# Optimization experiments

Hardware: AMD Instinct MI355X
Metric: run time of the kernel (lower is better)

## Reference

```python
import jax, jax.numpy as jnp
import numpy as np
from jax import lax

C, K, EMB = 10, 32, 32
B, H, W = 32, 128, 128
DIRS = ((-1, 0), (1, 0), (0, -1), (0, 1))  # up, down, left, right


def _shift(x, dh, dw):
    # shift (B,H,W,...) by (dh,dw) with zero fill; x[b,h,w] <- x[b,h+dh,w+dw]
    pad = [(0, 0), (max(dh, 0), max(-dh, 0)), (max(dw, 0), max(-dw, 0))] + [(0, 0)] * (x.ndim - 3)
    xp = jnp.pad(x, pad)
    h0, w0 = max(-dh, 0), max(-dw, 0)
    return lax.dynamic_slice_in_dim(lax.dynamic_slice_in_dim(xp, h0, x.shape[1], 1), w0, x.shape[2], 2)


def conv(x, w, b):
    y = lax.conv_general_dilated(x, w, (1, 1), 'SAME',
                                 dimension_numbers=('NHWC', 'HWIO', 'NHWC'))
    return y + b


def small_cnn(x, w1, b1, w2, b2, w3, b3):
    x = jax.nn.relu(conv(x, w1, b1))
    x = jax.nn.relu(conv(x, w2, b2))
    return conv(x, w3, b3)


def neighbor_affinity(phi, tau=0.5):
    # phi: (B,H,W,D) -> w: (B,H,W,4) Gaussian feature affinity to 4 neighbors
    ones = jnp.ones(phi.shape[:3] + (1,), phi.dtype)
    ws = []
    for dh, dw in DIRS:
        nb = _shift(phi, dh, dw)
        valid = _shift(ones, dh, dw)[..., 0]
        d2 = jnp.sum((phi - nb) ** 2, axis=-1)
        ws.append(jnp.exp(-d2 / tau) * valid)
    return jnp.stack(ws, axis=-1)


def init_seeds_soft(Bv, Hv, Wv, Kv, dtype=jnp.float32):
    # K seeds on a gh x gw grid; soft assignment by squared distance
    gh = 4
    gw = Kv // gh
    sh = (jnp.arange(gh, dtype=dtype) + 0.5) * (Hv / gh)
    sw = (jnp.arange(gw, dtype=dtype) + 0.5) * (Wv / gw)
    seed_h = jnp.repeat(sh, gw)  # (K,)
    seed_w = jnp.tile(sw, gh)    # (K,)
    hh = jnp.arange(Hv, dtype=dtype)[:, None, None]
    ww = jnp.arange(Wv, dtype=dtype)[None, :, None]
    d2 = (hh - seed_h) ** 2 + (ww - seed_w) ** 2  # (H,W,K)
    sigma2 = (Hv / gh) * (Wv / gw)
    A = jax.nn.softmax(-d2 / sigma2, axis=-1)
    return jnp.broadcast_to(A[None], (Bv, Hv, Wv, Kv))


def soft_message_pass(A, w, beta=2.0):
    # aggregate neighbor assignments weighted by affinity, renormalize over K
    agg = jnp.zeros_like(A)
    for d, (dh, dw) in enumerate(DIRS):
        agg = agg + w[..., d:d + 1] * _shift(A, dh, dw)
    return jax.nn.softmax(beta * agg, axis=-1)


def soft_pool_features(G, A):
    # G:(B,H,W,C), A:(B,H,W,K) -> T:(B,K,1+2+C+4)
    Bv, Hv, Wv, Cv = G.shape
    eps = 1e-6
    mass = jnp.sum(A, axis=(1, 2)) + eps                      # (B,K)
    hh = (jnp.arange(Hv, dtype=G.dtype) + 0.5) / Hv
    ww = (jnp.arange(Wv, dtype=G.dtype) + 0.5) / Wv
    h_c = jnp.einsum('bhwk,h->bk', A, hh) / mass
    w_c = jnp.einsum('bhwk,w->bk', A, ww) / mass
    col = jnp.einsum('bhwk,bhwc->bkc', A, G) / mass[..., None]
    h2 = jnp.einsum('bhwk,h->bk', A, hh ** 2) / mass
    w2 = jnp.einsum('bhwk,w->bk', A, ww ** 2) / mass
    h_sd = jnp.sqrt(jax.nn.relu(h2 - h_c ** 2) + eps)
    w_sd = jnp.sqrt(jax.nn.relu(w2 - w_c ** 2) + eps)
    size = (mass / (Hv * Wv))[..., None]                      # (B,K,1)
    cen = jnp.stack([h_c, w_c], axis=-1)                      # (B,K,2)
    bbox = jnp.stack([h_c - h_sd, h_c + h_sd, w_c - w_sd, w_c + w_sd], axis=-1)
    return jnp.concatenate([size, cen, col, bbox], axis=-1)


def setup_inputs() -> dict:
    key = jax.random.key(0)
    ks = jax.random.split(key, 4)
    X = jax.random.randint(ks[0], (B, H, W), 0, C)
    w1 = jax.random.normal(ks[1], (3, 3, C, 32), jnp.float32) * (1.0 / np.sqrt(9 * C))
    w2 = jax.random.normal(ks[2], (3, 3, 32, 32), jnp.float32) * (1.0 / np.sqrt(9 * 32))
    w3 = jax.random.normal(ks[3], (1, 1, 32, EMB), jnp.float32) * (1.0 / np.sqrt(32))
    return {'X': X, 'w1': w1, 'b1': jnp.zeros((32,), jnp.float32),
            'w2': w2, 'b2': jnp.zeros((32,), jnp.float32),
            'w3': w3, 'b3': jnp.zeros((EMB,), jnp.float32)}


def reference(X, w1, b1, w2, b2, w3, b3):
    G = jax.nn.one_hot(X, C, dtype=jnp.float32)              # (B,H,W,C)
    phi = small_cnn(G, w1, b1, w2, b2, w3, b3)               # (B,H,W,EMB)
    w = neighbor_affinity(phi)                               # (B,H,W,4)
    A = init_seeds_soft(G.shape[0], G.shape[1], G.shape[2], K, G.dtype)
    for _ in range(8):
        A = soft_message_pass(A, w, beta=2.0)
    T = soft_pool_features(G, A)
    return A, T
```

## Files before the change

kernel.cpp:

```cpp
#include <hip/hip_runtime.h>
#include <math.h>

#define HD 128
#define WD 128
#define BB 32
#define KK 32
#define NPIX (BB*HD*WD)
#define PLANE ((size_t)NPIX*8)

typedef _Float16 f16;
typedef __attribute__((ext_vector_type(8))) _Float16 f16x8;
typedef __attribute__((ext_vector_type(4))) float f32x4;

__device__ __forceinline__ int swz(int row, int g){
  return row*64 + (((g + (row >> 1)) & 3) << 4);
}

__device__ __forceinline__ float xexp2(float x){
#if __has_builtin(__builtin_amdgcn_exp2f)
  return __builtin_amdgcn_exp2f(x);
#else
  return exp2f(x);
#endif
}
__device__ __forceinline__ float xrcp(float x){
#if __has_builtin(__builtin_amdgcn_rcpf)
  return __builtin_amdgcn_rcpf(x);
#else
  return 1.f/x;
#endif
}
__device__ __forceinline__ f16x8 bc8(f16 x){
  f16x8 v;
  #pragma unroll
  for (int j = 0; j < 8; j++) v[j] = x;
  return v;
}

__global__ __launch_bounds__(512, 2) void cnn_kernel(
    const int* __restrict__ X,
    const float* __restrict__ w1, const float* __restrict__ b1,
    const float* __restrict__ w2, const float* __restrict__ b2,
    const float* __restrict__ w3, const float* __restrict__ b3,
    f16* __restrict__ phi)
{
  __shared__ f16 sW1f[9*11*40];
  __shared__ int   sX[20*36];
  __shared__ float sB2[32], sB3[32];
  __shared__ f16 x1[612*32];
  __shared__ f16 w2t[9*32*32];
  __shared__ f16 w3t[32*32];

  const int tid = threadIdx.x;
  const int img = blockIdx.z;
  const int bh0 = blockIdx.y * 16;
  const int bw0 = blockIdx.x * 32;

  for (int i = tid; i < 9*11*32; i += 512) {
    int tap = i / 352, c = (i % 352) >> 5, oc = i & 31;
    float v = (c < 10) ? w1[tap*320 + c*32 + oc] : 0.f;
    if (tap == 4 && c < 10) v += b1[oc];
    sW1f[(tap*11 + c)*40 + oc] = (f16)v;
  }
  for (int i = tid; i < 9*32*32; i += 512) {
    int tap = i >> 10, ic = (i >> 5) & 31, oc = i & 31;
    int off = swz(tap*32 + oc, ic >> 3) + (ic & 7)*2;
    *(f16*)((char*)w2t + off) = (f16)w2[i];
  }
  for (int i = tid; i < 32*32; i += 512) {
    int ic = i >> 5, oe = i & 31;
    int off = swz(oe, ic >> 3) + (ic & 7)*2;
    *(f16*)((char*)w3t + off) = (f16)w3[i];
  }
  if (tid < 32) { sB2[tid] = b2[tid]; sB3[tid] = b3[tid]; }
  for (int i = tid; i < 20*36; i += 512) {
    int ti = i / 36, tj = i % 36;
    int gh = bh0 - 2 + ti, gw = bw0 - 2 + tj;
    sX[i] = (gh >= 0 && gh < HD && gw >= 0 && gw < WD) ? X[(img*HD + gh)*WD + gw] : 10;
  }
  __syncthreads();

  for (int p = tid; p < 612; p += 512) {
    int hr = p / 34, hc = p - hr*34;
    int gh = bh0 + hr - 1, gw = bw0 + hc - 1;
    if (gh >= 0 && gh < HD && gw >= 0 && gw < WD) {
      f16x8 acc[4];
      {
        int c = sX[hr*36 + hc];
        const f16* wr = &sW1f[c*40];
        #pragma unroll
        for (int g = 0; g < 4; g++) acc[g] = *(const f16x8*)(wr + g*8);
      }
      #pragma unroll
      for (int tap = 1; tap < 9; tap++) {
        const int ti = tap/3, tj = tap%3;
        int c = sX[(hr+ti)*36 + hc + tj];
        const f16* wr = &sW1f[(tap*11 + c)*40];
        #pragma unroll
        for (int g = 0; g < 4; g++) acc[g] += *(const f16x8*)(wr + g*8);
      }
      #pragma unroll
      for (int g = 0; g < 4; g++) {
        f16x8 r = acc[g];
        #pragma unroll
        for (int j = 0; j < 8; j++) r[j] = (r[j] > (f16)0.f) ? r[j] : (f16)0.f;
        *(f16x8*)((char*)x1 + swz(p, g)) = r;
      }
    } else {
      f16x8 z;
      #pragma unroll
      for (int j = 0; j < 8; j++) z[j] = (f16)0.f;
      #pragma unroll
      for (int g = 0; g < 4; g++) *(f16x8*)((char*)x1 + swz(p, g)) = z;
    }
  }
  __syncthreads();

  const int lane = tid & 63;
  const int wv   = tid >> 6;
  const int lr   = lane & 15;
  const int kg   = lane >> 4;
  const int mts  = wv * 4;

  int arow0[4];
  #pragma unroll
  for (int q = 0; q < 4; q++) {
    int px = (mts + q)*16 + lr;
    arow0[q] = (px >> 5)*34 + (px & 31);
  }
  float b2v0 = sB2[lr], b2v1 = sB2[lr + 16];
  f32x4 acc[4][2];
  #pragma unroll
  for (int q = 0; q < 4; q++) {
    acc[q][0] = (f32x4){b2v0, b2v0, b2v0, b2v0};
    acc[q][1] = (f32x4){b2v1, b2v1, b2v1, b2v1};
  }
  #pragma unroll
  for (int tap = 0; tap < 9; tap++) {
    const int ti = tap/3, tj = tap%3;
    f16x8 bf0 = *(const f16x8*)((const char*)w2t + swz(tap*32 + lr,      kg));
    f16x8 bf1 = *(const f16x8*)((const char*)w2t + swz(tap*32 + lr + 16, kg));
    #pragma unroll
    for (int q = 0; q < 4; q++) {
      int row = arow0[q] + ti*34 + tj;
      f16x8 af = *(const f16x8*)((const char*)x1 + swz(row, kg));
      acc[q][0] = __builtin_amdgcn_mfma_f32_16x16x32_f16(af, bf0, acc[q][0], 0, 0, 0);
      acc[q][1] = __builtin_amdgcn_mfma_f32_16x16x32_f16(af, bf1, acc[q][1], 0, 0, 0);
    }
  }
  __syncthreads();

  #pragma unroll
  for (int q = 0; q < 4; q++)
    #pragma unroll
    for (int nt = 0; nt < 2; nt++) {
      int oc = nt*16 + lr;
      #pragma unroll
      for (int rg = 0; rg < 4; rg++) {
        int px = (mts + q)*16 + kg*4 + rg;
        int off = swz(px, oc >> 3) + (oc & 7)*2;
        *(f16*)((char*)x1 + off) = (f16)fmaxf(acc[q][nt][rg], 0.f);
      }
    }
  __syncthreads();

  {
    f16x8 cf0 = *(const f16x8*)((const char*)w3t + swz(lr,      kg));
    f16x8 cf1 = *(const f16x8*)((const char*)w3t + swz(lr + 16, kg));
    float b3v0 = sB3[lr], b3v1 = sB3[lr + 16];
    #pragma unroll
    for (int q = 0; q < 4; q++) {
      f16x8 af = *(const f16x8*)((const char*)x1 + swz((mts + q)*16 + lr, kg));
      f32x4 o0 = (f32x4){b3v0, b3v0, b3v0, b3v0};
      f32x4 o1 = (f32x4){b3v1, b3v1, b3v1, b3v1};
      o0 = __builtin_amdgcn_mfma_f32_16x16x32_f16(af, cf0, o0, 0, 0, 0);
      o1 = __builtin_amdgcn_mfma_f32_16x16x32_f16(af, cf1, o1, 0, 0, 0);
      #pragma unroll
      for (int rg = 0; rg < 4; rg++) {
        int px = (mts + q)*16 + kg*4 + rg;
        int gh = bh0 + (px >> 5), gw = bw0 + (px & 31);
        f16* dst = phi + ((size_t)((img*HD + gh)*WD + gw))*32;
        dst[lr]      = (f16)o0[rg];
        dst[lr + 16] = (f16)o1[rg];
      }
    }
  }
}

#define WSCALE 2.8853900817779268f

__device__ __forceinline__ float aff_lds(const f16* __restrict__ sphi, int slot,
                                         f16x8 c0, f16x8 c1, f16x8 c2, f16x8 c3,
                                         bool valid) {
  f16x8 n0 = *(const f16x8*)((const char*)sphi + swz(slot, 0));
  f16x8 n1 = *(const f16x8*)((const char*)sphi + swz(slot, 1));
  f16x8 n2 = *(const f16x8*)((const char*)sphi + swz(slot, 2));
  f16x8 n3 = *(const f16x8*)((const char*)sphi + swz(slot, 3));
  f16x8 d0 = c0 - n0; f16x8 s = d0*d0;
  f16x8 d1 = c1 - n1; s += d1*d1;
  f16x8 d2 = c2 - n2; s += d2*d2;
  f16x8 d3 = c3 - n3; s += d3*d3;
  float d2f = 0.f;
  #pragma unroll
  for (int j = 0; j < 8; j++) d2f += (float)s[j];
  return valid ? WSCALE * xexp2(-WSCALE * d2f) : 0.f;
}

__global__ __launch_bounds__(256, 4) void aff_kernel(const f16* __restrict__ phi, float* __restrict__ wb) {
  __shared__ f16 sphi[612*32];

  const int blk  = blockIdx.x;
  const int tile = blk & 31;
  const int img  = blk >> 5;
  const int th0  = (tile >> 2) * 16;
  const int tw0  = (tile & 3) * 32;
  const size_t ibase = (size_t)img * HD * WD;

  for (int task = threadIdx.x; task < 2448; task += 256) {
    int p = task >> 2, g = task & 3;
    int r = p / 34, c = p - r*34;
    int gh = min(max(th0 - 1 + r, 0), HD-1);
    int gw = min(max(tw0 - 1 + c, 0), WD-1);
    f16x8 v = *(const f16x8*)(phi + (ibase + gh*WD + gw)*32 + g*8);
    *(f16x8*)((char*)sphi + swz(p, g)) = v;
  }
  __syncthreads();

  for (int p2 = threadIdx.x; p2 < 512; p2 += 256) {
    int r2 = p2 >> 5, c2 = p2 & 31;
    int gh = th0 + r2, gw = tw0 + c2;
    int qc = (r2+1)*34 + (c2+1);
    f16x8 c0 = *(const f16x8*)((const char*)sphi + swz(qc, 0));
    f16x8 c1 = *(const f16x8*)((const char*)sphi + swz(qc, 1));
    f16x8 c2v = *(const f16x8*)((const char*)sphi + swz(qc, 2));
    f16x8 c3 = *(const f16x8*)((const char*)sphi + swz(qc, 3));
    float4 out;
    out.x = aff_lds(sphi, qc + 34, c0,c1,c2v,c3, gh < HD-1);
    out.y = aff_lds(sphi, qc - 34, c0,c1,c2v,c3, gh > 0);
    out.z = aff_lds(sphi, qc + 1,  c0,c1,c2v,c3, gw < WD-1);
    out.w = aff_lds(sphi, qc - 1,  c0,c1,c2v,c3, gw > 0);
    ((float4*)wb)[ibase + gh*WD + gw] = out;
  }
}

__device__ __forceinline__ void a0_accum2(float* a, int hh, int ww, float wt) {
  const float C = 0.0028177637517362567f;
  float eh[4], ew[8];
  float sh = 0.f, sw = 0.f;
  const float fh = (float)hh, fw = (float)ww;
  #pragma unroll
  for (int kh = 0; kh < 4; kh++) { float d = fh - (float)(kh*32+16); eh[kh] = xexp2(-d*d*C); sh += eh[kh]; }
  #pragma unroll
  for (int kw = 0; kw < 8; kw++) { float d = fw - (float)(kw*16+8); ew[kw] = xexp2(-d*d*C); sw += ew[kw]; }
  float sc = wt * xrcp(sh * sw);
  #pragma unroll
  for (int kh = 0; kh < 4; kh++) {
    float ehs = eh[kh] * sc;
    #pragma unroll
    for (int kw = 0; kw < 8; kw++) a[kh*8+kw] = fmaf(ehs, ew[kw], a[kh*8+kw]);
  }
}

template<int FIRST>
__global__ __launch_bounds__(256, 6) void mp2_kernel(const f16* __restrict__ Ain,
                                                     const float* __restrict__ wb,
                                                     f16* __restrict__ Aout) {
  __shared__ f16 amid[340*32];

  const int blk  = blockIdx.x;
  const int xcd  = blk & 7;
  const int q    = blk >> 3;
  const int img  = xcd + ((q >> 6) << 3);
  const int tile = q & 63;
  const int th0  = (tile >> 2) * 8;
  const int tw0  = (tile & 3) * 32;
  const size_t ibase = (size_t)img * HD * WD;

  for (int p = threadIdx.x; p < 340; p += 256) {
    int r = p / 34, cc = p - r*34;
    int gh = th0 - 1 + r, gw = tw0 - 1 + cc;
    bool inimg = ((unsigned)gh < (unsigned)HD) && ((unsigned)gw < (unsigned)WD);
    int ghc = min(max(gh, 0), HD-1), gwc = min(max(gw, 0), WD-1);
    float4 wd = inimg ? ((const float4*)wb)[ibase + gh*WD + gw] : make_float4(0.f,0.f,0.f,0.f);
    int hu = ghc + ((ghc < HD-1) ? 1 : 0);
    int hd = ghc - ((ghc > 0)    ? 1 : 0);
    int wl = gwc + ((gwc < WD-1) ? 1 : 0);
    int wr = gwc - ((gwc > 0)    ? 1 : 0);

    float s = 0.f;
    f16x8 pe[4];
    if (FIRST) {
      float a[32];
      #pragma unroll
      for (int k = 0; k < 32; k++) a[k] = 0.f;
      a0_accum2(a, hu, gwc, wd.x);
      a0_accum2(a, hd, gwc, wd.y);
      a0_accum2(a, ghc, wl, wd.z);
      a0_accum2(a, ghc, wr, wd.w);
      #pragma unroll
      for (int g = 0; g < 4; g++)
        #pragma unroll
        for (int j = 0; j < 8; j++) { float e = xexp2(a[g*8+j]); s += e; pe[g][j] = (f16)e; }
    } else {
      const size_t iu_ = ibase + (size_t)hu*WD + gwc;
      const size_t id_ = ibase + (size_t)hd*WD + gwc;
      const size_t il_ = ibase + (size_t)ghc*WD + wl;
      const size_t ir_ = ibase + (size_t)ghc*WD + wr;
      f16x8 w0 = bc8((f16)wd.x), w1 = bc8((f16)wd.y), w2 = bc8((f16)wd.z), w3 = bc8((f16)wd.w);
      #pragma unroll
      for (int g = 0; g < 4; g++) {
        const f16* pg = Ain + (size_t)g*PLANE;
        f16x8 v0 = *(const f16x8*)(pg + iu_*8);
        f16x8 v1 = *(const f16x8*)(pg + id_*8);
        f16x8 v2 = *(const f16x8*)(pg + il_*8);
        f16x8 v3 = *(const f16x8*)(pg + ir_*8);
        f16x8 agg = v0*w0 + v1*w1 + v2*w2 + v3*w3;
        #pragma unroll
        for (int j = 0; j < 8; j++) { float e = xexp2((float)agg[j]); s += e; pe[g][j] = (f16)e; }
      }
    }
    f16x8 iv = bc8((f16)xrcp(s));
    #pragma unroll
    for (int g = 0; g < 4; g++)
      *(f16x8*)((char*)amid + swz(p, g)) = pe[g]*iv;
  }
  __syncthreads();

  {
    int r2 = threadIdx.x >> 5, c2 = threadIdx.x & 31;
    int gh = th0 + r2, gw = tw0 + c2;
    int rm = r2 + 1, cm = c2 + 1;
    float4 wd = ((const float4*)wb)[ibase + gh*WD + gw];
    int q0 = (rm + ((gh < HD-1) ? 1 : 0))*34 + cm;
    int q1 = (rm - ((gh > 0)    ? 1 : 0))*34 + cm;
    int q2 = rm*34 + cm + ((gw < WD-1) ? 1 : 0);
    int q3 = rm*34 + cm - ((gw > 0)    ? 1 : 0);
    f16x8 w0 = bc8((f16)wd.x), w1 = bc8((f16)wd.y), w2 = bc8((f16)wd.z), w3 = bc8((f16)wd.w);
    float s = 0.f;
    f16x8 pe[4];
    #pragma unroll
    for (int g = 0; g < 4; g++) {
      f16x8 v0 = *(const f16x8*)((const char*)amid + swz(q0, g));
      f16x8 v1 = *(const f16x8*)((const char*)amid + swz(q1, g));
      f16x8 v2 = *(const f16x8*)((const char*)amid + swz(q2, g));
      f16x8 v3 = *(const f16x8*)((const char*)amid + swz(q3, g));
      f16x8 agg = v0*w0 + v1*w1 + v2*w2 + v3*w3;
      #pragma unroll
      for (int j = 0; j < 8; j++) { float e = xexp2((float)agg[j]); s += e; pe[g][j] = (f16)e; }
    }
    f16x8 iv = bc8((f16)xrcp(s));
    size_t opix = ibase + (size_t)gh*WD + gw;
    #pragma unroll
    for (int g = 0; g < 4; g++)
      *(f16x8*)(Aout + (size_t)g*PLANE + opix*8) = pe[g]*iv;
  }
}

__global__ __launch_bounds__(256) void conv_kernel(const f16* __restrict__ Ap,
                                                   float* __restrict__ Aout) {
  const int t = blockIdx.x * 256 + threadIdx.x;
  const int px = t >> 2, g = t & 3;
  f16x8 v = *(const f16x8*)(Ap + (size_t)g*PLANE + (size_t)px*8);
  float4 o0, o1;
  o0.x = (float)v[0]; o0.y = (float)v[1]; o0.z = (float)v[2]; o0.w = (float)v[3];
  o1.x = (float)v[4]; o1.y = (float)v[5]; o1.z = (float)v[6]; o1.w = (float)v[7];
  float4* dst = (float4*)(Aout + (size_t)px*32 + g*8);
  dst[0] = o0; dst[1] = o1;
}

__global__ __launch_bounds__(256) void pool1_kernel(const f16* __restrict__ Ap,
                                                    const int* __restrict__ X,
                                                    float* __restrict__ part) {
  const int b = blockIdx.x, cy = blockIdx.y;
  const int k = threadIdx.x & 31, sub = threadIdx.x >> 5;
  const int h = cy*4 + (sub >> 1);
  const int w0 = (sub & 1) * 64;
  const float hh = ((float)h + 0.5f) * (1.f/128.f);
  float s0 = 0.f, sw = 0.f, sw2 = 0.f;
  float col[10];
  #pragma unroll
  for (int c = 0; c < 10; c++) col[c] = 0.f;
  const f16* pl = Ap + (size_t)(k >> 3)*PLANE + ((size_t)((b*HD + h)*WD + w0))*8 + (k & 7);
  const int* Xrow = X + (b*HD + h)*WD + w0;
  for (int w = 0; w < 64; w++) {
    float a  = (float)pl[w*8];
    float ww = ((float)(w + w0) + 0.5f) * (1.f/128.f);
    s0 += a; sw = fmaf(ww, a, sw); sw2 = fmaf(ww*ww, a, sw2);
    int x = Xrow[w];
    #pragma unroll
    for (int c = 0; c < 10; c++) col[c] += (x == c) ? a : 0.f;
  }
  __shared__ float red[8][32][15];
  float vals[15];
  vals[0] = s0; vals[1] = hh*s0; vals[2] = sw; vals[3] = hh*hh*s0; vals[4] = sw2;
  #pragma unroll
  for (int c = 0; c < 10; c++) vals[5+c] = col[c];
  #pragma unroll
  for (int q = 0; q < 15; q++) red[sub][k][q] = vals[q];
  __syncthreads();
  if (sub == 0) {
    #pragma unroll
    for (int q = 0; q < 15; q++) {
      float v = 0.f;
      #pragma unroll
      for (int s2 = 0; s2 < 8; s2++) v += red[s2][k][q];
      part[(((size_t)b*32 + cy)*32 + k)*15 + q] = v;
    }
  }
}

__global__ __launch_bounds__(256) void pool2_kernel(const float* __restrict__ part,
                                                    float* __restrict__ T) {
  const int t = blockIdx.x * 256 + threadIdx.x;
  if (t >= BB*KK) return;
  const int b = t >> 5, k = t & 31;
  float s[15];
  #pragma unroll
  for (int q = 0; q < 15; q++) s[q] = 0.f;
  for (int cy = 0; cy < 32; cy++) {
    const float* p = part + (((size_t)b*32 + cy)*32 + k)*15;
    #pragma unroll
    for (int q = 0; q < 15; q++) s[q] += p[q];
  }
  float mass = s[0] + 1e-6f;
  float inv  = 1.f / mass;
  float h_c = s[1]*inv, w_c = s[2]*inv, h2 = s[3]*inv, w2 = s[4]*inv;
  float h_sd = sqrtf(fmaxf(h2 - h_c*h_c, 0.f) + 1e-6f);
  float w_sd = sqrtf(fmaxf(w2 - w_c*w_c, 0.f) + 1e-6f);
  float* o = T + (size_t)t*17;
  o[0] = mass * (1.f/16384.f);
  o[1] = h_c; o[2] = w_c;
  #pragma unroll
  for (int c = 0; c < 10; c++) o[3+c] = s[5+c]*inv;
  o[13] = h_c - h_sd; o[14] = h_c + h_sd; o[15] = w_c - w_sd; o[16] = w_c + w_sd;
}

extern "C" void kernel_launch(void* const* d_in, const int* in_sizes, int n_in,
                              void* d_out, int out_size, void* d_ws, size_t ws_size,
                              hipStream_t stream) {
  const int*   X  = (const int*)d_in[0];
  const float* w1 = (const float*)d_in[1];
  const float* b1 = (const float*)d_in[2];
  const float* w2 = (const float*)d_in[3];
  const float* b2 = (const float*)d_in[4];
  const float* w3 = (const float*)d_in[5];
  const float* b3 = (const float*)d_in[6];

  float* out   = (float*)d_out;
  float* A_out = out;
  float* T_out = out + (size_t)NPIX * KK;

  char*  ws   = (char*)d_ws;
  f16*   bufA = (f16*)ws;
  f16*   bufB = (f16*)(ws + (size_t)32*1024*1024);
  float* wb   = (float*)(ws + (size_t)64*1024*1024);
  float* part = (float*)ws;

  f16* phi = bufB;
  cnn_kernel<<<dim3(WD/32, HD/16, BB), 512, 0, stream>>>(X, w1, b1, w2, b2, w3, b3, phi);
  aff_kernel<<<1024, 256, 0, stream>>>(phi, wb);

  mp2_kernel<1><<<2048, 256, 0, stream>>>(nullptr, wb, bufA);
  mp2_kernel<0><<<2048, 256, 0, stream>>>(bufA, wb, bufB);
  mp2_kernel<0><<<2048, 256, 0, stream>>>(bufB, wb, bufA);
  mp2_kernel<0><<<2048, 256, 0, stream>>>(bufA, wb, bufB);

  conv_kernel<<<NPIX*4/256, 256, 0, stream>>>(bufB, A_out);
  pool1_kernel<<<dim3(BB, 32), 256, 0, stream>>>(bufB, X, part);
  pool2_kernel<<<(BB*KK + 255)/256, 256, 0, stream>>>(part, T_out);
}
```

Before: 269.8 us.

## Fuse CNN with affinity, fuse fp32 output conversion into last message pass

```diff
diff --git a/kernel.cpp b/kernel.cpp
--- a/kernel.cpp
+++ b/kernel.cpp
@@ -10,6 +10,7 @@
 
 typedef _Float16 f16;
 typedef __attribute__((ext_vector_type(8))) _Float16 f16x8;
+typedef __attribute__((ext_vector_type(4))) _Float16 f16x4;
 typedef __attribute__((ext_vector_type(4))) float f32x4;
 
 __device__ __forceinline__ int swz(int row, int g){
@@ -37,17 +38,19 @@
   return v;
 }
 
-__global__ __launch_bounds__(512, 2) void cnn_kernel(
+#define WSCALE 2.8853900817779268f
+
+__global__ __launch_bounds__(512, 4) void cnnaff_kernel(
     const int* __restrict__ X,
     const float* __restrict__ w1, const float* __restrict__ b1,
     const float* __restrict__ w2, const float* __restrict__ b2,
     const float* __restrict__ w3, const float* __restrict__ b3,
-    f16* __restrict__ phi)
+    float* __restrict__ wb)
 {
   __shared__ f16 sW1f[9*11*40];
-  __shared__ int   sX[20*36];
+  __shared__ int   sX[22*38];
   __shared__ float sB2[32], sB3[32];
-  __shared__ f16 x1[612*32];
+  __shared__ f16 x1[720*32];
   __shared__ f16 w2t[9*32*32];
   __shared__ f16 w3t[32*32];
 
@@ -73,38 +76,38 @@
     *(f16*)((char*)w3t + off) = (f16)w3[i];
   }
   if (tid < 32) { sB2[tid] = b2[tid]; sB3[tid] = b3[tid]; }
-  for (int i = tid; i < 20*36; i += 512) {
-    int ti = i / 36, tj = i % 36;
-    int gh = bh0 - 2 + ti, gw = bw0 - 2 + tj;
+  for (int i = tid; i < 22*38; i += 512) {
+    int ti = i / 38, tj = i % 38;
+    int gh = bh0 - 3 + ti, gw = bw0 - 3 + tj;
     sX[i] = (gh >= 0 && gh < HD && gw >= 0 && gw < WD) ? X[(img*HD + gh)*WD + gw] : 10;
   }
   __syncthreads();
 
-  for (int p = tid; p < 612; p += 512) {
-    int hr = p / 34, hc = p - hr*34;
-    int gh = bh0 + hr - 1, gw = bw0 + hc - 1;
+  for (int p = tid; p < 720; p += 512) {
+    int r = p / 36, c = p - r*36;
+    int gh = bh0 - 2 + r, gw = bw0 - 2 + c;
     if (gh >= 0 && gh < HD && gw >= 0 && gw < WD) {
       f16x8 acc[4];
       {
-        int c = sX[hr*36 + hc];
-        const f16* wr = &sW1f[c*40];
+        int cc = sX[r*38 + c];
+        const f16* wr = &sW1f[cc*40];
         #pragma unroll
         for (int g = 0; g < 4; g++) acc[g] = *(const f16x8*)(wr + g*8);
       }
       #pragma unroll
       for (int tap = 1; tap < 9; tap++) {
         const int ti = tap/3, tj = tap%3;
-        int c = sX[(hr+ti)*36 + hc + tj];
-        const f16* wr = &sW1f[(tap*11 + c)*40];
+        int cc = sX[(r+ti)*38 + c + tj];
+        const f16* wr = &sW1f[(tap*11 + cc)*40];
         #pragma unroll
         for (int g = 0; g < 4; g++) acc[g] += *(const f16x8*)(wr + g*8);
       }
       #pragma unroll
       for (int g = 0; g < 4; g++) {
-        f16x8 r = acc[g];
+        f16x8 rr = acc[g];
         #pragma unroll
-        for (int j = 0; j < 8; j++) r[j] = (r[j] > (f16)0.f) ? r[j] : (f16)0.f;
-        *(f16x8*)((char*)x1 + swz(p, g)) = r;
+        for (int j = 0; j < 8; j++) rr[j] = (rr[j] > (f16)0.f) ? rr[j] : (f16)0.f;
+        *(f16x8*)((char*)x1 + swz(p, g)) = rr;
       }
     } else {
       f16x8 z;
@@ -120,18 +123,19 @@
   const int wv   = tid >> 6;
   const int lr   = lane & 15;
   const int kg   = lane >> 4;
-  const int mts  = wv * 4;
-
-  int arow0[4];
-  #pragma unroll
-  for (int q = 0; q < 4; q++) {
+  const int mts  = wv * 5;
+
+  int arow0[5];
+  #pragma unroll
+  for (int q = 0; q < 5; q++) {
     int px = (mts + q)*16 + lr;
-    arow0[q] = (px >> 5)*34 + (px & 31);
+    int pr = px / 34, pc = px - pr*34;
+    arow0[q] = pr*36 + pc;
   }
   float b2v0 = sB2[lr], b2v1 = sB2[lr + 16];
-  f32x4 acc[4][2];
-  #pragma unroll
-  for (int q = 0; q < 4; q++) {
+  f32x4 acc[5][2];
+  #pragma unroll
+  for (int q = 0; q < 5; q++) {
     acc[q][0] = (f32x4){b2v0, b2v0, b2v0, b2v0};
     acc[q][1] = (f32x4){b2v1, b2v1, b2v1, b2v1};
   }
@@ -141,8 +145,8 @@
     f16x8 bf0 = *(const f16x8*)((const char*)w2t + swz(tap*32 + lr,      kg));
     f16x8 bf1 = *(const f16x8*)((const char*)w2t + swz(tap*32 + lr + 16, kg));
     #pragma unroll
-    for (int q = 0; q < 4; q++) {
-      int row = arow0[q] + ti*34 + tj;
+    for (int q = 0; q < 5; q++) {
+      int row = arow0[q] + ti*36 + tj;
       f16x8 af = *(const f16x8*)((const char*)x1 + swz(row, kg));
       acc[q][0] = __builtin_amdgcn_mfma_f32_16x16x32_f16(af, bf0, acc[q][0], 0, 0, 0);
       acc[q][1] = __builtin_amdgcn_mfma_f32_16x16x32_f16(af, bf1, acc[q][1], 0, 0, 0);
@@ -151,7 +155,7 @@
   __syncthreads();
 
   #pragma unroll
-  for (int q = 0; q < 4; q++)
+  for (int q = 0; q < 5; q++)
     #pragma unroll
     for (int nt = 0; nt < 2; nt++) {
       int oc = nt*16 + lr;
@@ -169,7 +173,7 @@
     f16x8 cf1 = *(const f16x8*)((const char*)w3t + swz(lr + 16, kg));
     float b3v0 = sB3[lr], b3v1 = sB3[lr + 16];
     #pragma unroll
-    for (int q = 0; q < 4; q++) {
+    for (int q = 0; q < 5; q++) {
       f16x8 af = *(const f16x8*)((const char*)x1 + swz((mts + q)*16 + lr, kg));
       f32x4 o0 = (f32x4){b3v0, b3v0, b3v0, b3v0};
       f32x4 o1 = (f32x4){b3v1, b3v1, b3v1, b3v1};
@@ -178,68 +182,43 @@
       #pragma unroll
       for (int rg = 0; rg < 4; rg++) {
         int px = (mts + q)*16 + kg*4 + rg;
-        int gh = bh0 + (px >> 5), gw = bw0 + (px & 31);
-        f16* dst = phi + ((size_t)((img*HD + gh)*WD + gw))*32;
-        dst[lr]      = (f16)o0[rg];
-        dst[lr + 16] = (f16)o1[rg];
-      }
-    }
-  }
-}
-
-#define WSCALE 2.8853900817779268f
-
-__device__ __forceinline__ float aff_lds(const f16* __restrict__ sphi, int slot,
-                                         f16x8 c0, f16x8 c1, f16x8 c2, f16x8 c3,
-                                         bool valid) {
-  f16x8 n0 = *(const f16x8*)((const char*)sphi + swz(slot, 0));
-  f16x8 n1 = *(const f16x8*)((const char*)sphi + swz(slot, 1));
-  f16x8 n2 = *(const f16x8*)((const char*)sphi + swz(slot, 2));
-  f16x8 n3 = *(const f16x8*)((const char*)sphi + swz(slot, 3));
-  f16x8 d0 = c0 - n0; f16x8 s = d0*d0;
-  f16x8 d1 = c1 - n1; s += d1*d1;
-  f16x8 d2 = c2 - n2; s += d2*d2;
-  f16x8 d3 = c3 - n3; s += d3*d3;
-  float d2f = 0.f;
-  #pragma unroll
-  for (int j = 0; j < 8; j++) d2f += (float)s[j];
-  return valid ? WSCALE * xexp2(-WSCALE * d2f) : 0.f;
-}
-
-__global__ __launch_bounds__(256, 4) void aff_kernel(const f16* __restrict__ phi, float* __restrict__ wb) {
-  __shared__ f16 sphi[612*32];
-
-  const int blk  = blockIdx.x;
-  const int tile = blk & 31;
-  const int img  = blk >> 5;
-  const int th0  = (tile >> 2) * 16;
-  const int tw0  = (tile & 3) * 32;
-  const size_t ibase = (size_t)img * HD * WD;
-
-  for (int task = threadIdx.x; task < 2448; task += 256) {
-    int p = task >> 2, g = task & 3;
-    int r = p / 34, c = p - r*34;
-    int gh = min(max(th0 - 1 + r, 0), HD-1);
-    int gw = min(max(tw0 - 1 + c, 0), WD-1);
-    f16x8 v = *(const f16x8*)(phi + (ibase + gh*WD + gw)*32 + g*8);
-    *(f16x8*)((char*)sphi + swz(p, g)) = v;
-  }
-  __syncthreads();
-
-  for (int p2 = threadIdx.x; p2 < 512; p2 += 256) {
-    int r2 = p2 >> 5, c2 = p2 & 31;
-    int gh = th0 + r2, gw = tw0 + c2;
+        int offA = swz(px, lr >> 3) + (lr & 7)*2;
+        int offB = swz(px, (lr+16) >> 3) + (lr & 7)*2;
+        *(f16*)((char*)x1 + offA) = (f16)o0[rg];
+        *(f16*)((char*)x1 + offB) = (f16)o1[rg];
+      }
+    }
+  }
+  __syncthreads();
+
+  {
+    int r2 = tid >> 5, c2 = tid & 31;
+    int gh = bh0 + r2, gw = bw0 + c2;
     int qc = (r2+1)*34 + (c2+1);
-    f16x8 c0 = *(const f16x8*)((const char*)sphi + swz(qc, 0));
-    f16x8 c1 = *(const f16x8*)((const char*)sphi + swz(qc, 1));
-    f16x8 c2v = *(const f16x8*)((const char*)sphi + swz(qc, 2));
-    f16x8 c3 = *(const f16x8*)((const char*)sphi + swz(qc, 3));
+    f16x8 c0 = *(const f16x8*)((const char*)x1 + swz(qc, 0));
+    f16x8 c1 = *(const f16x8*)((const char*)x1 + swz(qc, 1));
+    f16x8 c2v = *(const f16x8*)((const char*)x1 + swz(qc, 2));
+    f16x8 c3 = *(const f16x8*)((const char*)x1 + swz(qc, 3));
     float4 out;
-    out.x = aff_lds(sphi, qc + 34, c0,c1,c2v,c3, gh < HD-1);
-    out.y = aff_lds(sphi, qc - 34, c0,c1,c2v,c3, gh > 0);
-    out.z = aff_lds(sphi, qc + 1,  c0,c1,c2v,c3, gw < WD-1);
-    out.w = aff_lds(sphi, qc - 1,  c0,c1,c2v,c3, gw > 0);
-    ((float4*)wb)[ibase + gh*WD + gw] = out;
+    #pragma unroll
+    for (int d = 0; d < 4; d++) {
+      int slot = (d == 0) ? qc + 34 : (d == 1) ? qc - 34 : (d == 2) ? qc + 1 : qc - 1;
+      bool valid = (d == 0) ? (gh < HD-1) : (d == 1) ? (gh > 0) : (d == 2) ? (gw < WD-1) : (gw > 0);
+      f16x8 n0 = *(const f16x8*)((const char*)x1 + swz(slot, 0));
+      f16x8 n1 = *(const f16x8*)((const char*)x1 + swz(slot, 1));
+      f16x8 n2 = *(const f16x8*)((const char*)x1 + swz(slot, 2));
+      f16x8 n3 = *(const f16x8*)((const char*)x1 + swz(slot, 3));
+      f16x8 d0 = c0 - n0; f16x8 s = d0*d0;
+      f16x8 d1 = c1 - n1; s += d1*d1;
+      f16x8 d2 = c2v - n2; s += d2*d2;
+      f16x8 d3 = c3 - n3; s += d3*d3;
+      float d2f = 0.f;
+      #pragma unroll
+      for (int j = 0; j < 8; j++) d2f += (float)s[j];
+      float v = valid ? WSCALE * xexp2(-WSCALE * d2f) : 0.f;
+      if (d == 0) out.x = v; else if (d == 1) out.y = v; else if (d == 2) out.z = v; else out.w = v;
+    }
+    ((float4*)wb)[(size_t)img*HD*WD + gh*WD + gw] = out;
   }
 }
 
@@ -261,22 +240,23 @@
   }
 }
 
-template<int FIRST>
-__global__ __launch_bounds__(256, 6) void mp2_kernel(const f16* __restrict__ Ain,
+template<int FIRST, int LAST>
+__global__ __launch_bounds__(512, 6) void mp2_kernel(const f16* __restrict__ Ain,
                                                      const float* __restrict__ wb,
-                                                     f16* __restrict__ Aout) {
-  __shared__ f16 amid[340*32];
+                                                     f16* __restrict__ Aout,
+                                                     float* __restrict__ AoutF) {
+  __shared__ f16 amid[612*32];
 
   const int blk  = blockIdx.x;
   const int xcd  = blk & 7;
   const int q    = blk >> 3;
-  const int img  = xcd + ((q >> 6) << 3);
-  const int tile = q & 63;
-  const int th0  = (tile >> 2) * 8;
+  const int img  = xcd + ((q >> 5) << 3);
+  const int tile = q & 31;
+  const int th0  = (tile >> 2) * 16;
   const int tw0  = (tile & 3) * 32;
   const size_t ibase = (size_t)img * HD * WD;
 
-  for (int p = threadIdx.x; p < 340; p += 256) {
+  for (int p = threadIdx.x; p < 612; p += 512) {
     int r = p / 34, cc = p - r*34;
     int gh = th0 - 1 + r, gw = tw0 - 1 + cc;
     bool inimg = ((unsigned)gh < (unsigned)HD) && ((unsigned)gw < (unsigned)WD);
@@ -349,26 +329,41 @@
       for (int j = 0; j < 8; j++) { float e = xexp2((float)agg[j]); s += e; pe[g][j] = (f16)e; }
     }
     f16x8 iv = bc8((f16)xrcp(s));
-    size_t opix = ibase + (size_t)gh*WD + gw;
-    #pragma unroll
-    for (int g = 0; g < 4; g++)
-      *(f16x8*)(Aout + (size_t)g*PLANE + opix*8) = pe[g]*iv;
-  }
-}
-
-__global__ __launch_bounds__(256) void conv_kernel(const f16* __restrict__ Ap,
-                                                   float* __restrict__ Aout) {
-  const int t = blockIdx.x * 256 + threadIdx.x;
-  const int px = t >> 2, g = t & 3;
-  f16x8 v = *(const f16x8*)(Ap + (size_t)g*PLANE + (size_t)px*8);
-  float4 o0, o1;
-  o0.x = (float)v[0]; o0.y = (float)v[1]; o0.z = (float)v[2]; o0.w = (float)v[3];
-  o1.x = (float)v[4]; o1.y = (float)v[5]; o1.z = (float)v[6]; o1.w = (float)v[7];
-  float4* dst = (float4*)(Aout + (size_t)px*32 + g*8);
-  dst[0] = o0; dst[1] = o1;
-}
-
-__global__ __launch_bounds__(256) void pool1_kernel(const f16* __restrict__ Ap,
+    #pragma unroll
+    for (int g = 0; g < 4; g++) pe[g] = pe[g]*iv;
+
+    if (!LAST) {
+      size_t opix = ibase + (size_t)gh*WD + gw;
+      #pragma unroll
+      for (int g = 0; g < 4; g++)
+        *(f16x8*)(Aout + (size_t)g*PLANE + opix*8) = pe[g];
+    } else {
+      __syncthreads();
+      f16* planes = amid;
+      #pragma unroll
+      for (int g = 0; g < 4; g++)
+        *(f16x8*)((char*)planes + (g*513 + threadIdx.x)*16) = pe[g];
+      __syncthreads();
+      float* obase = AoutF + ((size_t)(img*HD + th0)*WD + tw0)*32;
+      #pragma unroll
+      for (int rep = 0; rep < 8; rep++) {
+        int flat = rep*512 + threadIdx.x;
+        int row = flat >> 8;
+        int within = flat & 255;
+        int pxr = within >> 3;
+        int kq = within & 7;
+        int g = kq >> 1, half = kq & 1;
+        int pxl = row*32 + pxr;
+        f16x4 v = *(const f16x4*)((const char*)planes + (g*513 + pxl)*16 + half*8);
+        float4 o;
+        o.x = (float)v[0]; o.y = (float)v[1]; o.z = (float)v[2]; o.w = (float)v[3];
+        *(float4*)(obase + (size_t)row*WD*32 + pxr*32 + kq*4) = o;
+      }
+    }
+  }
+}
+
+__global__ __launch_bounds__(256) void pool1_kernel(const float* __restrict__ A,
                                                     const int* __restrict__ X,
                                                     float* __restrict__ part) {
   const int b = blockIdx.x, cy = blockIdx.y;
@@ -380,10 +375,10 @@
   float col[10];
   #pragma unroll
   for (int c = 0; c < 10; c++) col[c] = 0.f;
-  const f16* pl = Ap + (size_t)(k >> 3)*PLANE + ((size_t)((b*HD + h)*WD + w0))*8 + (k & 7);
-  const int* Xrow = X + (b*HD + h)*WD + w0;
+  const float* Arow = A + ((size_t)((b*HD + h)*WD + w0))*32 + k;
+  const int*   Xrow = X + (b*HD + h)*WD + w0;
   for (int w = 0; w < 64; w++) {
-    float a  = (float)pl[w*8];
+    float a  = Arow[(size_t)w*32];
     float ww = ((float)(w + w0) + 0.5f) * (1.f/128.f);
     s0 += a; sw = fmaf(ww, a, sw); sw2 = fmaf(ww*ww, a, sw2);
     int x = Xrow[w];
@@ -456,16 +451,13 @@
   float* wb   = (float*)(ws + (size_t)64*1024*1024);
   float* part = (float*)ws;
 
-  f16* phi = bufB;
-  cnn_kernel<<<dim3(WD/32, HD/16, BB), 512, 0, stream>>>(X, w1, b1, w2, b2, w3, b3, phi);
-  aff_kernel<<<1024, 256, 0, stream>>>(phi, wb);
-
-  mp2_kernel<1><<<2048, 256, 0, stream>>>(nullptr, wb, bufA);
-  mp2_kernel<0><<<2048, 256, 0, stream>>>(bufA, wb, bufB);
-  mp2_kernel<0><<<2048, 256, 0, stream>>>(bufB, wb, bufA);
-  mp2_kernel<0><<<2048, 256, 0, stream>>>(bufA, wb, bufB);
-
-  conv_kernel<<<NPIX*4/256, 256, 0, stream>>>(bufB, A_out);
-  pool1_kernel<<<dim3(BB, 32), 256, 0, stream>>>(bufB, X, part);
+  cnnaff_kernel<<<dim3(WD/32, HD/16, BB), 512, 0, stream>>>(X, w1, b1, w2, b2, w3, b3, wb);
+
+  mp2_kernel<1,0><<<1024, 512, 0, stream>>>(nullptr, wb, bufA, nullptr);
+  mp2_kernel<0,0><<<1024, 512, 0, stream>>>(bufA, wb, bufB, nullptr);
+  mp2_kernel<0,0><<<1024, 512, 0, stream>>>(bufB, wb, bufA, nullptr);
+  mp2_kernel<0,1><<<1024, 512, 0, stream>>>(bufA, wb, nullptr, A_out);
+
+  pool1_kernel<<<dim3(BB, 32), 256, 0, stream>>>(A_out, X, part);
   pool2_kernel<<<(BB*KK + 255)/256, 256, 0, stream>>>(part, T_out);
 }
```

Result: faster. 236.2 us (-12.5%).

## Fuse final message pass with fp32 output conversion and pooling partials

Applied to the files above, without the earlier changes.

```diff
diff --git a/kernel.cpp b/kernel.cpp
--- a/kernel.cpp
+++ b/kernel.cpp
@@ -10,6 +10,7 @@
 
 typedef _Float16 f16;
 typedef __attribute__((ext_vector_type(8))) _Float16 f16x8;
+typedef __attribute__((ext_vector_type(4))) _Float16 f16x4;
 typedef __attribute__((ext_vector_type(4))) float f32x4;
 
 __device__ __forceinline__ int swz(int row, int g){
@@ -36,6 +37,8 @@
   for (int j = 0; j < 8; j++) v[j] = x;
   return v;
 }
+
+#define WSCALE 2.8853900817779268f
 
 __global__ __launch_bounds__(512, 2) void cnn_kernel(
     const int* __restrict__ X,
@@ -186,8 +189,6 @@
     }
   }
 }
-
-#define WSCALE 2.8853900817779268f
 
 __device__ __forceinline__ float aff_lds(const f16* __restrict__ sphi, int slot,
                                          f16x8 c0, f16x8 c1, f16x8 c2, f16x8 c3,
@@ -262,21 +263,21 @@
 }
 
 template<int FIRST>
-__global__ __launch_bounds__(256, 6) void mp2_kernel(const f16* __restrict__ Ain,
+__global__ __launch_bounds__(512, 6) void mp2_kernel(const f16* __restrict__ Ain,
                                                      const float* __restrict__ wb,
                                                      f16* __restrict__ Aout) {
-  __shared__ f16 amid[340*32];
+  __shared__ f16 amid[612*32];
 
   const int blk  = blockIdx.x;
   const int xcd  = blk & 7;
   const int q    = blk >> 3;
-  const int img  = xcd + ((q >> 6) << 3);
-  const int tile = q & 63;
-  const int th0  = (tile >> 2) * 8;
+  const int img  = xcd + ((q >> 5) << 3);
+  const int tile = q & 31;
+  const int th0  = (tile >> 2) * 16;
   const int tw0  = (tile & 3) * 32;
   const size_t ibase = (size_t)img * HD * WD;
 
-  for (int p = threadIdx.x; p < 340; p += 256) {
+  for (int p = threadIdx.x; p < 612; p += 512) {
     int r = p / 34, cc = p - r*34;
     int gh = th0 - 1 + r, gw = tw0 - 1 + cc;
     bool inimg = ((unsigned)gh < (unsigned)HD) && ((unsigned)gw < (unsigned)WD);
@@ -356,56 +357,147 @@
   }
 }
 
-__global__ __launch_bounds__(256) void conv_kernel(const f16* __restrict__ Ap,
-                                                   float* __restrict__ Aout) {
-  const int t = blockIdx.x * 256 + threadIdx.x;
-  const int px = t >> 2, g = t & 3;
-  f16x8 v = *(const f16x8*)(Ap + (size_t)g*PLANE + (size_t)px*8);
-  float4 o0, o1;
-  o0.x = (float)v[0]; o0.y = (float)v[1]; o0.z = (float)v[2]; o0.w = (float)v[3];
-  o1.x = (float)v[4]; o1.y = (float)v[5]; o1.z = (float)v[6]; o1.w = (float)v[7];
-  float4* dst = (float4*)(Aout + (size_t)px*32 + g*8);
-  dst[0] = o0; dst[1] = o1;
-}
-
-__global__ __launch_bounds__(256) void pool1_kernel(const f16* __restrict__ Ap,
-                                                    const int* __restrict__ X,
-                                                    float* __restrict__ part) {
-  const int b = blockIdx.x, cy = blockIdx.y;
-  const int k = threadIdx.x & 31, sub = threadIdx.x >> 5;
-  const int h = cy*4 + (sub >> 1);
-  const int w0 = (sub & 1) * 64;
-  const float hh = ((float)h + 0.5f) * (1.f/128.f);
-  float s0 = 0.f, sw = 0.f, sw2 = 0.f;
-  float col[10];
-  #pragma unroll
-  for (int c = 0; c < 10; c++) col[c] = 0.f;
-  const f16* pl = Ap + (size_t)(k >> 3)*PLANE + ((size_t)((b*HD + h)*WD + w0))*8 + (k & 7);
-  const int* Xrow = X + (b*HD + h)*WD + w0;
-  for (int w = 0; w < 64; w++) {
-    float a  = (float)pl[w*8];
-    float ww = ((float)(w + w0) + 0.5f) * (1.f/128.f);
-    s0 += a; sw = fmaf(ww, a, sw); sw2 = fmaf(ww*ww, a, sw2);
-    int x = Xrow[w];
-    #pragma unroll
-    for (int c = 0; c < 10; c++) col[c] += (x == c) ? a : 0.f;
-  }
-  __shared__ float red[8][32][15];
-  float vals[15];
-  vals[0] = s0; vals[1] = hh*s0; vals[2] = sw; vals[3] = hh*hh*s0; vals[4] = sw2;
-  #pragma unroll
-  for (int c = 0; c < 10; c++) vals[5+c] = col[c];
-  #pragma unroll
-  for (int q = 0; q < 15; q++) red[sub][k][q] = vals[q];
-  __syncthreads();
-  if (sub == 0) {
-    #pragma unroll
-    for (int q = 0; q < 15; q++) {
-      float v = 0.f;
-      #pragma unroll
-      for (int s2 = 0; s2 < 8; s2++) v += red[s2][k][q];
-      part[(((size_t)b*32 + cy)*32 + k)*15 + q] = v;
-    }
+__global__ __launch_bounds__(512, 2) void mp2last_kernel(const f16* __restrict__ Ain,
+                                                         const float* __restrict__ wb,
+                                                         const int* __restrict__ X,
+                                                         float* __restrict__ AoutF,
+                                                         float* __restrict__ part) {
+  __shared__ f16 amid[612*32];
+  __shared__ float red[16*33*15];
+  __shared__ int sXt[512];
+
+  const int blk  = blockIdx.x;
+  const int xcd  = blk & 7;
+  const int q    = blk >> 3;
+  const int img  = xcd + ((q >> 5) << 3);
+  const int tile = q & 31;
+  const int th0  = (tile >> 2) * 16;
+  const int tw0  = (tile & 3) * 32;
+  const size_t ibase = (size_t)img * HD * WD;
+
+  {
+    int r = threadIdx.x >> 5, c = threadIdx.x & 31;
+    sXt[threadIdx.x] = X[ibase + (size_t)(th0 + r)*WD + tw0 + c];
+  }
+
+  for (int p = threadIdx.x; p < 612; p += 512) {
+    int r = p / 34, cc = p - r*34;
+    int gh = th0 - 1 + r, gw = tw0 - 1 + cc;
+    bool inimg = ((unsigned)gh < (unsigned)HD) && ((unsigned)gw < (unsigned)WD);
+    int ghc = min(max(gh, 0), HD-1), gwc = min(max(gw, 0), WD-1);
+    float4 wd = inimg ? ((const float4*)wb)[ibase + gh*WD + gw] : make_float4(0.f,0.f,0.f,0.f);
+    int hu = ghc + ((ghc < HD-1) ? 1 : 0);
+    int hd = ghc - ((ghc > 0)    ? 1 : 0);
+    int wl = gwc + ((gwc < WD-1) ? 1 : 0);
+    int wr = gwc - ((gwc > 0)    ? 1 : 0);
+
+    const size_t iu_ = ibase + (size_t)hu*WD + gwc;
+    const size_t id_ = ibase + (size_t)hd*WD + gwc;
+    const size_t il_ = ibase + (size_t)ghc*WD + wl;
+    const size_t ir_ = ibase + (size_t)ghc*WD + wr;
+    f16x8 w0 = bc8((f16)wd.x), w1 = bc8((f16)wd.y), w2 = bc8((f16)wd.z), w3 = bc8((f16)wd.w);
+    float s = 0.f;
+    f16x8 pe[4];
+    #pragma unroll
+    for (int g = 0; g < 4; g++) {
+      const f16* pg = Ain + (size_t)g*PLANE;
+      f16x8 v0 = *(const f16x8*)(pg + iu_*8);
+      f16x8 v1 = *(const f16x8*)(pg + id_*8);
+      f16x8 v2 = *(const f16x8*)(pg + il_*8);
+      f16x8 v3 = *(const f16x8*)(pg + ir_*8);
+      f16x8 agg = v0*w0 + v1*w1 + v2*w2 + v3*w3;
+      #pragma unroll
+      for (int j = 0; j < 8; j++) { float e = xexp2((float)agg[j]); s += e; pe[g][j] = (f16)e; }
+    }
+    f16x8 iv = bc8((f16)xrcp(s));
+    #pragma unroll
+    for (int g = 0; g < 4; g++)
+      *(f16x8*)((char*)amid + swz(p, g)) = pe[g]*iv;
+  }
+  __syncthreads();
+
+  f16x8 pe[4];
+  {
+    int r2 = threadIdx.x >> 5, c2 = threadIdx.x & 31;
+    int gh = th0 + r2, gw = tw0 + c2;
+    int rm = r2 + 1, cm = c2 + 1;
+    float4 wd = ((const float4*)wb)[ibase + gh*WD + gw];
+    int q0 = (rm + ((gh < HD-1) ? 1 : 0))*34 + cm;
+    int q1 = (rm - ((gh > 0)    ? 1 : 0))*34 + cm;
+    int q2 = rm*34 + cm + ((gw < WD-1) ? 1 : 0);
+    int q3 = rm*34 + cm - ((gw > 0)    ? 1 : 0);
+    f16x8 w0 = bc8((f16)wd.x), w1 = bc8((f16)wd.y), w2 = bc8((f16)wd.z), w3 = bc8((f16)wd.w);
+    float s = 0.f;
+    #pragma unroll
+    for (int g = 0; g < 4; g++) {
+      f16x8 v0 = *(const f16x8*)((const char*)amid + swz(q0, g));
+      f16x8 v1 = *(const f16x8*)((const char*)amid + swz(q1, g));
+      f16x8 v2 = *(const f16x8*)((const char*)amid + swz(q2, g));
+      f16x8 v3 = *(const f16x8*)((const char*)amid + swz(q3, g));
+      f16x8 agg = v0*w0 + v1*w1 + v2*w2 + v3*w3;
+      #pragma unroll
+      for (int j = 0; j < 8; j++) { float e = xexp2((float)agg[j]); s += e; pe[g][j] = (f16)e; }
+    }
+    f16x8 iv = bc8((f16)xrcp(s));
+    #pragma unroll
+    for (int g = 0; g < 4; g++) pe[g] = pe[g]*iv;
+  }
+
+  __syncthreads();
+  f16* planes = amid;
+  #pragma unroll
+  for (int g = 0; g < 4; g++)
+    *(f16x8*)((char*)planes + (g*513 + threadIdx.x)*16) = pe[g];
+  __syncthreads();
+  {
+    float* obase = AoutF + ((size_t)(img*HD + th0)*WD + tw0)*32;
+    #pragma unroll
+    for (int rep = 0; rep < 8; rep++) {
+      int flat = rep*512 + threadIdx.x;
+      int row = flat >> 8;
+      int within = flat & 255;
+      int pxr = within >> 3;
+      int kq = within & 7;
+      int g = kq >> 1, half = kq & 1;
+      int pxl = row*32 + pxr;
+      f16x4 v = *(const f16x4*)((const char*)planes + (g*513 + pxl)*16 + half*8);
+      float4 o;
+      o.x = (float)v[0]; o.y = (float)v[1]; o.z = (float)v[2]; o.w = (float)v[3];
+      *(float4*)(obase + (size_t)row*WD*32 + pxr*32 + kq*4) = o;
+    }
+  }
+
+  {
+    const int k  = threadIdx.x & 31;
+    const int gr = threadIdx.x >> 5;
+    const int gq = k >> 3, j = k & 7;
+    const float hh = ((float)(th0 + gr) + 0.5f) * (1.f/128.f);
+    float s0 = 0.f, sw = 0.f, sw2 = 0.f;
+    float col[10];
+    #pragma unroll
+    for (int c = 0; c < 10; c++) col[c] = 0.f;
+    #pragma unroll
+    for (int i = 0; i < 32; i++) {
+      int px = gr*32 + i;
+      float a = (float)*(const f16*)((const char*)planes + (gq*513 + px)*16 + j*2);
+      float ww = ((float)(tw0 + i) + 0.5f) * (1.f/128.f);
+      s0 += a; sw = fmaf(ww, a, sw); sw2 = fmaf(ww*ww, a, sw2);
+      int x = sXt[px];
+      #pragma unroll
+      for (int c = 0; c < 10; c++) col[c] += (x == c) ? a : 0.f;
+    }
+    float* rd = &red[(gr*33 + k)*15];
+    rd[0] = s0; rd[1] = hh*s0; rd[2] = sw; rd[3] = hh*hh*s0; rd[4] = sw2;
+    #pragma unroll
+    for (int c = 0; c < 10; c++) rd[5+c] = col[c];
+  }
+  __syncthreads();
+  if (threadIdx.x < 480) {
+    int k = threadIdx.x / 15, qq = threadIdx.x - k*15;
+    float v = 0.f;
+    #pragma unroll
+    for (int g = 0; g < 16; g++) v += red[(g*33 + k)*15 + qq];
+    part[(((size_t)img*32 + tile)*32 + k)*15 + qq] = v;
   }
 }
 
@@ -454,18 +546,16 @@
   f16*   bufA = (f16*)ws;
   f16*   bufB = (f16*)(ws + (size_t)32*1024*1024);
   float* wb   = (float*)(ws + (size_t)64*1024*1024);
-  float* part = (float*)ws;
+  float* part = (float*)(ws + (size_t)72*1024*1024);
 
   f16* phi = bufB;
   cnn_kernel<<<dim3(WD/32, HD/16, BB), 512, 0, stream>>>(X, w1, b1, w2, b2, w3, b3, phi);
   aff_kernel<<<1024, 256, 0, stream>>>(phi, wb);
 
-  mp2_kernel<1><<<2048, 256, 0, stream>>>(nullptr, wb, bufA);
-  mp2_kernel<0><<<2048, 256, 0, stream>>>(bufA, wb, bufB);
-  mp2_kernel<0><<<2048, 256, 0, stream>>>(bufB, wb, bufA);
-  mp2_kernel<0><<<2048, 256, 0, stream>>>(bufA, wb, bufB);
-
-  conv_kernel<<<NPIX*4/256, 256, 0, stream>>>(bufB, A_out);
-  pool1_kernel<<<dim3(BB, 32), 256, 0, stream>>>(bufB, X, part);
+  mp2_kernel<1><<<1024, 512, 0, stream>>>(nullptr, wb, bufA);
+  mp2_kernel<0><<<1024, 512, 0, stream>>>(bufA, wb, bufB);
+  mp2_kernel<0><<<1024, 512, 0, stream>>>(bufB, wb, bufA);
+  mp2last_kernel<<<1024, 512, 0, stream>>>(bufA, wb, X, A_out, part);
+
   pool2_kernel<<<(BB*KK + 255)/256, 256, 0, stream>>>(part, T_out);
 }
```

Measured after the change: 234.2 us. 13.2% less time.
